# Performance work log

Hardware: AMD Instinct MI355X
Metric: run time of the kernel (lower is better)

## Reference

```python
import jax, jax.numpy as jnp
import numpy as np

H = 96
W = 96
FX = 96.0
FY = 96.0
NEAR = 0.3
EPS = 1e-8


def q2r(quat):
    # quat: [N,4] (w,x,y,z) -> [N,3,3]
    q = quat / (jnp.linalg.norm(quat, axis=-1, keepdims=True) + 1e-12)
    w, x, y, z = q[:, 0], q[:, 1], q[:, 2], q[:, 3]
    R = jnp.stack([
        1 - 2 * (y * y + z * z), 2 * (x * y - w * z), 2 * (x * z + w * y),
        2 * (x * y + w * z), 1 - 2 * (x * x + z * z), 2 * (y * z - w * x),
        2 * (x * z - w * y), 2 * (y * z + w * x), 1 - 2 * (x * x + y * y),
    ], axis=-1).reshape(-1, 3, 3)
    return R


def setup_inputs() -> dict:
    key = jax.random.key(0)
    ks = jax.random.split(key, 8)
    N = 4096
    pos_xy = jax.random.uniform(ks[0], (N, 2), minval=-2.0, maxval=2.0, dtype=jnp.float32)
    pos_z = jax.random.uniform(ks[1], (N, 1), minval=2.0, maxval=6.0, dtype=jnp.float32)
    pos = jnp.concatenate([pos_xy, pos_z], axis=-1)
    rgb = jax.random.normal(ks[2], (N, 3), dtype=jnp.float32)
    opa = jax.random.normal(ks[3], (N,), dtype=jnp.float32)
    quat = jax.random.normal(ks[4], (N, 4), dtype=jnp.float32)
    scale = jax.random.uniform(ks[5], (N, 3), dtype=jnp.float32) * 0.05 + 0.005
    rot = jnp.eye(3, dtype=jnp.float32)
    tran = jnp.zeros(3, dtype=jnp.float32)
    return {"pos": pos, "rgb": rgb, "opa": opa, "quat": quat, "scale": scale, "rot": rot, "tran": tran}


def reference(pos, rgb, opa, quat, scale, rot, tran):
    # ---- project: world -> camera -> image space ----
    cam = pos @ rot.T + tran[None, :]              # [N,3]
    x, y, z = cam[:, 0], cam[:, 1], cam[:, 2]
    r = jnp.linalg.norm(cam, axis=-1)              # depth = ray length (camera_to_image)
    mean2d = jnp.stack([x / z, y / z], axis=-1)    # [N,2]

    # jacobian of (x/z, y/z, |p|) wrt camera-space point, [N,3,3]
    zeros = jnp.zeros_like(z)
    J = jnp.stack([
        1.0 / z, zeros, -x / (z * z),
        zeros, 1.0 / z, -y / (z * z),
        x / r, y / r, z / r,
    ], axis=-1).reshape(-1, 3, 3)

    # ---- 3D covariance: R S S^T R^T ----
    R = q2r(quat)                                   # [N,3,3]
    s = jnp.abs(scale) + 1e-4                       # [N,3]
    RS = R * s[:, None, :]                          # R @ diag(s)
    cov3d = jnp.einsum('nij,nkj->nik', RS, RS)      # [N,3,3]

    # ---- 2D covariance: (J W) cov3d (J W)^T, upper-left 2x2 ----
    JW = jnp.einsum('nij,jk->nik', J, rot)          # [N,3,3]
    cov2d = jnp.einsum('nij,njk,nlk->nil', JW, cov3d, JW)[:, :2, :2]  # [N,2,2]

    a = cov2d[:, 0, 0] + EPS
    d = cov2d[:, 1, 1] + EPS
    b = 0.5 * (cov2d[:, 0, 1] + cov2d[:, 1, 0])
    det = a * d - b * b
    inv_a = d / det
    inv_b = -b / det
    inv_d = a / det

    rgb_act = jax.nn.sigmoid(rgb)                   # [N,3]
    opa_act = jax.nn.sigmoid(opa)                   # [N]

    # ---- per-pixel gaussian evaluation in normalized image space ----
    u = (jnp.arange(W, dtype=jnp.float32) + 0.5 - W / 2) / FX   # [W]
    v = (jnp.arange(H, dtype=jnp.float32) + 0.5 - H / 2) / FY   # [H]
    pu = jnp.tile(u, H)                                          # [P]
    pv = jnp.repeat(v, W)                                        # [P]

    dx = pu[None, :] - mean2d[:, 0:1]               # [N,P]
    dy = pv[None, :] - mean2d[:, 1:2]               # [N,P]
    power = -0.5 * (inv_a[:, None] * dx * dx + 2.0 * inv_b[:, None] * dx * dy + inv_d[:, None] * dy * dy)
    alpha = opa_act[:, None] * jnp.exp(power)       # [N,P]
    alpha = jnp.clip(alpha, 0.0, 0.99)
    valid = (z > NEAR).astype(alpha.dtype)[:, None]
    alpha = alpha * valid

    # ---- depth-sorted alpha compositing ----
    order = jnp.argsort(r)                          # near -> far
    alpha_s = alpha[order]                          # [N,P]
    rgb_s = rgb_act[order]                          # [N,3]

    log_1m = jnp.log1p(-alpha_s)                    # [N,P]
    cum = jnp.cumsum(log_1m, axis=0)
    logT = jnp.concatenate([jnp.zeros((1, alpha_s.shape[1]), alpha_s.dtype), cum[:-1]], axis=0)
    w = jnp.exp(logT) * alpha_s                     # [N,P] blending weights
    img = jnp.einsum('np,nc->pc', w, rgb_s)         # [P,3]
    return img.reshape(H, W, 3)
```

## Files before the change

kernel.cpp:

```cpp
#include <hip/hip_runtime.h>
#include <math.h>

#define N_G   4096
#define IMW   96
#define TILE  6
#define TILES_X 16
#define NTILE (TILES_X*TILES_X)
#define NTHR  1024
#define NW    (NTHR/64)
#define NST   (N_G/NTHR)
#define NPX   (TILE*TILE)
#define NSEG  16
#define BCAP  2048
#define CAP   512
#define FXI   (1.0f/96.0f)
#define NEARP 0.3f
#define EPSV  1e-8f
#define LOG2E 1.4426950408889634f
#define LN2   0.6931471805599453f
#define CULL_K 26.0f

typedef unsigned long long ull;
typedef __attribute__((ext_vector_type(2))) unsigned long long ull2;

__global__ __launch_bounds__(NTHR, 1) void splat_k(
    const float* __restrict__ pos, const float* __restrict__ rgb,
    const float* __restrict__ opa, const float* __restrict__ quat,
    const float* __restrict__ scale, const float* __restrict__ rot,
    const float* __restrict__ tran, float* __restrict__ out)
{
    __shared__ unsigned int bl[BCAP];
    __shared__ __align__(16) ull skey[CAP+2];
    __shared__ int sslot[CAP];
    __shared__ float4 g0[CAP], g1[CAP];
    __shared__ float  g2[CAP];
    __shared__ float4 pix[NSEG*NPX];
    __shared__ int psum[4][CAP];
    __shared__ int bcnt_sh, cnt_sh;

    const int t = threadIdx.x;
    const int tile = blockIdx.x;
    const int tx = tile % TILES_X, ty = tile / TILES_X;
    const float u0 = ((float)(tx*TILE) + 0.5f - 48.0f) * FXI;
    const float u1 = u0 + (TILE-1) * FXI;
    const float v0 = ((float)(ty*TILE) + 0.5f - 48.0f) * FXI;
    const float v1 = v0 + (TILE-1) * FXI;
    const int wid = t >> 6, lane = t & 63;

    if (t == 0) { bcnt_sh = 0; cnt_sh = 0; }

    float R00=rot[0],R01=rot[1],R02=rot[2];
    float R10=rot[3],R11=rot[4],R12=rot[5];
    float R20=rot[6],R21=rot[7],R22=rot[8];
    float t0=tran[0], t1=tran[1], t2=tran[2];

    float pp0[NST], pp1[NST], pp2[NST], po[NST], ps0[NST], ps1[NST], ps2[NST];
    #pragma unroll
    for (int st = 0; st < NST; st++) {
        int gi = st*NTHR + t;
        pp0[st]=pos[gi*3+0]; pp1[st]=pos[gi*3+1]; pp2[st]=pos[gi*3+2];
        po[st]=opa[gi];
        ps0[st]=scale[gi*3+0]; ps1[st]=scale[gi*3+1]; ps2[st]=scale[gi*3+2];
    }
    __syncthreads();

    #pragma unroll
    for (int st = 0; st < NST; st++) {
        int gi = st*NTHR + t;
        float x = R00*pp0[st] + R01*pp1[st] + R02*pp2[st] + t0;
        float y = R10*pp0[st] + R11*pp1[st] + R12*pp2[st] + t1;
        float z = R20*pp0[st] + R21*pp1[st] + R22*pp2[st] + t2;
        float invz = 1.0f/z;
        float mu = x*invz, mv = y*invz;

        float inz2 = invz*invz;
        float fn = 2.0f*inz2 + (x*x + y*y)*inz2*inz2;
        float smax = fmaxf(fmaxf(fabsf(ps0[st]), fabsf(ps1[st])), fabsf(ps2[st])) + 1e-4f;
        float lmax = fn*smax*smax + EPSV;
        float amp = CULL_K + 1.0f + fminf(0.0f, po[st]*LOG2E);
        float r2b = amp * lmax * (2.0f*LN2) * 1.02f;

        float cu = fminf(fmaxf(mu, u0), u1);
        float cv = fminf(fmaxf(mv, v0), v1);
        float ddx = mu - cu, ddy = mv - cv;
        bool flag = (z > NEARP) && (amp > 0.0f) && (ddx*ddx + ddy*ddy <= r2b);

        ull m = __ballot(flag);
        int nm = __popcll(m);
        int base = 0;
        if (lane == 0 && nm) base = atomicAdd(&bcnt_sh, nm);
        base = __shfl(base, 0);
        if (flag) {
            int p = base + __popcll(m & ((1ull << lane) - 1ull));
            if (p < BCAP) bl[p] = (unsigned int)gi;
        }
    }
    __syncthreads();
    int bcnt = bcnt_sh; if (bcnt > BCAP) bcnt = BCAP;

    for (int s0i = 0; s0i < bcnt; s0i += NTHR) {
        int s = s0i + t;
        bool flag = false;
        float4 o0, o1; float ocb = 0.0f, rr = 0.0f;
        unsigned int gi = 0;
        if (s < bcnt) {
            gi = bl[s];
            float p0=pos[gi*3+0], p1=pos[gi*3+1], p2=pos[gi*3+2];
            float x = R00*p0 + R01*p1 + R02*p2 + t0;
            float y = R10*p0 + R11*p1 + R12*p2 + t1;
            float z = R20*p0 + R21*p1 + R22*p2 + t2;
            rr = sqrtf(x*x + y*y + z*z);
            float invz = 1.0f/z;
            float mu = x*invz, mv = y*invz;

            float J02 = -x*invz*invz, J12 = -y*invz*invz;
            float JW00 = invz*R00 + J02*R20;
            float JW01 = invz*R01 + J02*R21;
            float JW02 = invz*R02 + J02*R22;
            float JW10 = invz*R10 + J12*R20;
            float JW11 = invz*R11 + J12*R21;
            float JW12 = invz*R12 + J12*R22;

            float qw=quat[gi*4+0], qx=quat[gi*4+1], qy=quat[gi*4+2], qz=quat[gi*4+3];
            float qn = sqrtf(qw*qw+qx*qx+qy*qy+qz*qz) + 1e-12f;
            float qi = 1.0f/qn;
            qw*=qi; qx*=qi; qy*=qi; qz*=qi;
            float Q00=1.f-2.f*(qy*qy+qz*qz), Q01=2.f*(qx*qy-qw*qz), Q02=2.f*(qx*qz+qw*qy);
            float Q10=2.f*(qx*qy+qw*qz), Q11=1.f-2.f*(qx*qx+qz*qz), Q12=2.f*(qy*qz-qw*qx);
            float Q20=2.f*(qx*qz-qw*qy), Q21=2.f*(qy*qz+qw*qx), Q22=1.f-2.f*(qx*qx+qy*qy);

            float sa=fabsf(scale[gi*3+0])+1e-4f;
            float sb=fabsf(scale[gi*3+1])+1e-4f;
            float sc=fabsf(scale[gi*3+2])+1e-4f;
            float A00=Q00*sa,A01=Q01*sb,A02=Q02*sc;
            float A10=Q10*sa,A11=Q11*sb,A12=Q12*sc;
            float A20=Q20*sa,A21=Q21*sb,A22=Q22*sc;
            float C00=A00*A00+A01*A01+A02*A02;
            float C01=A00*A10+A01*A11+A02*A12;
            float C02=A00*A20+A01*A21+A02*A22;
            float C11=A10*A10+A11*A11+A12*A12;
            float C12=A10*A20+A11*A21+A12*A22;
            float C22=A20*A20+A21*A21+A22*A22;
            float M00=JW00*C00+JW01*C01+JW02*C02;
            float M01=JW00*C01+JW01*C11+JW02*C12;
            float M02=JW00*C02+JW01*C12+JW02*C22;
            float M10=JW10*C00+JW11*C01+JW12*C02;
            float M11=JW10*C01+JW11*C11+JW12*C12;
            float M12=JW10*C02+JW11*C12+JW12*C22;
            float a  = M00*JW00+M01*JW01+M02*JW02 + EPSV;
            float d  = M10*JW10+M11*JW11+M12*JW12 + EPSV;
            float bb = 0.5f*((M00*JW10+M01*JW11+M02*JW12)+(M10*JW00+M11*JW01+M12*JW02));
            float invdet = 1.0f/(a*d - bb*bb);
            float iaP = -0.5f*d*invdet*LOG2E;
            float ibP =  bb*invdet*LOG2E;
            float idP = -0.5f*a*invdet*LOG2E;

            float sig_o = 1.0f/(1.0f+__expf(-opa[gi]));
            float opa_eff = (z > NEARP) ? sig_o : 0.0f;

            float q00 = -iaP, q01 = -0.5f*ibP, q11 = -idP;
            float df = q00 - q11;
            float lam = 0.5f*((q00 + q11) - sqrtf(df*df + 4.0f*q01*q01));
            lam = fmaxf(lam, 1e-20f);
            float r2 = (CULL_K + log2f(opa_eff)) / lam;

            float cu = fminf(fmaxf(mu, u0), u1);
            float cv = fminf(fmaxf(mv, v0), v1);
            float ddx = mu - cu, ddy = mv - cv;
            flag = (ddx*ddx + ddy*ddy) <= r2;

            if (flag) {
                float c0 = 1.0f/(1.0f+__expf(-rgb[gi*3+0]));
                float c1 = 1.0f/(1.0f+__expf(-rgb[gi*3+1]));
                float c2 = 1.0f/(1.0f+__expf(-rgb[gi*3+2]));
                o0 = make_float4(mu, mv, iaP, ibP);
                o1 = make_float4(idP, opa_eff, c0, c1);
                ocb = c2;
            }
        }
        ull m = __ballot(flag);
        int nm = __popcll(m);
        int base = 0;
        if (lane == 0 && nm) base = atomicAdd(&cnt_sh, nm);
        base = __shfl(base, 0);
        if (flag) {
            int p = base + __popcll(m & ((1ull << lane) - 1ull));
            if (p < CAP) {
                g0[p] = o0; g1[p] = o1; g2[p] = ocb;
                skey[p] = ((ull)__float_as_uint(rr) << 32) | gi;
            }
        }
    }
    __syncthreads();
    int cnt = cnt_sh; if (cnt > CAP) cnt = CAP;

    if (t == 0 && (cnt & 1)) skey[cnt] = ~0ull;
    __syncthreads();
    int cnt2 = cnt + (cnt & 1);
    int nq = cnt2 >> 1;
    const ull2* sk2 = (const ull2*)skey;
    ull v = 0;
    bool small = (cnt <= 256);
    if (small) {
        const int g = t >> 8, e = t & 255;
        if (e < cnt) {
            v = skey[e];
            int wA = (nq * g) >> 2;
            int wB = (nq * (g+1)) >> 2;
            int c = 0;
            for (int w = wA; w < wB; w++) {
                ull2 p = sk2[w];
                c += (p.x < v) ? 1 : 0;
                c += (p.y < v) ? 1 : 0;
            }
            psum[g][e] = c;
        }
    } else {
        const int g = t >> 9, e = t & 511;
        if (e < cnt) {
            v = skey[e];
            int wA = (nq * g) >> 1;
            int wB = (nq * (g+1)) >> 1;
            int c = 0;
            for (int w = wA; w < wB; w++) {
                ull2 p = sk2[w];
                c += (p.x < v) ? 1 : 0;
                c += (p.y < v) ? 1 : 0;
            }
            psum[g][e] = c;
        }
    }
    __syncthreads();
    if (t < cnt) {
        int r = small ? (psum[0][t] + psum[1][t] + psum[2][t] + psum[3][t])
                      : (psum[0][t] + psum[1][t]);
        skey[r]  = v;
        sslot[r] = t;
    }
    __syncthreads();

    {
        const int seg = wid;
        const bool act = (lane < NPX);
        const int pid = act ? lane : 0;
        const int px = tx*TILE + (pid % TILE);
        const int py = ty*TILE + (pid / TILE);
        const float pu = ((float)px + 0.5f - 48.0f) * FXI;
        const float pv = ((float)py + 0.5f - 48.0f) * FXI;

        const int per = (cnt + NSEG - 1) / NSEG;
        const int sA = min(seg * per, cnt);
        const int sB = min(sA + per, cnt);

        float T = 1.0f, cr = 0.0f, cg = 0.0f, cb = 0.0f;
        for (int s = sA; s < sB; s++) {
            int slot = sslot[s];
            float4 a0 = g0[slot];
            float4 a1 = g1[slot];
            float  a2 = g2[slot];
            float dx = pu - a0.x;
            float dy = pv - a0.y;
            float pw = dx*(a0.z*dx + a0.w*dy) + a1.x*dy*dy;
            float al = fminf(a1.y * __builtin_amdgcn_exp2f(pw), 0.99f);
            float w = T * al;
            cr += w * a1.z;
            cg += w * a1.w;
            cb += w * a2;
            T *= (1.0f - al);
        }
        if (act) pix[seg*NPX + pid] = make_float4(cr, cg, cb, T);
    }
    __syncthreads();

    if (t < NPX) {
        float orr = 0.0f, og = 0.0f, ob = 0.0f, T2 = 1.0f;
        #pragma unroll
        for (int s = 0; s < NSEG; s++) {
            float4 P = pix[s*NPX + t];
            orr += T2 * P.x;
            og  += T2 * P.y;
            ob  += T2 * P.z;
            T2  *= P.w;
        }
        int px = tx*TILE + (t % TILE);
        int py = ty*TILE + (t / TILE);
        int pixel = py * IMW + px;
        out[pixel*3+0] = orr;
        out[pixel*3+1] = og;
        out[pixel*3+2] = ob;
    }
}

extern "C" void kernel_launch(void* const* d_in, const int* in_sizes, int n_in,
                              void* d_out, int out_size, void* d_ws, size_t ws_size,
                              hipStream_t stream) {
    const float* pos   = (const float*)d_in[0];
    const float* rgb   = (const float*)d_in[1];
    const float* opa   = (const float*)d_in[2];
    const float* quat  = (const float*)d_in[3];
    const float* scale = (const float*)d_in[4];
    const float* rot   = (const float*)d_in[5];
    const float* tran  = (const float*)d_in[6];
    float* out = (float*)d_out;

    splat_k<<<NTILE, NTHR, 0, stream>>>(pos, rgb, opa, quat, scale, rot, tran, out);
}
```

Baseline: 14.22 us.

## Cull gaussians with exact ellipse bounding box and unify rank sort

The tile culling test now compares the per-axis extent of each gaussian's ellipse (from the quadratic form's determinant) against the per-axis distance to the tile. This replaces the circle bounded by the smallest eigenvalue, dropping a sqrt and keeping fewer elongated gaussians per tile. The counting rank sort now always uses four partial-sum groups, with each thread ranking two keys, replacing the two-mode small/large branch. This trades more compare work per thread for a better split of the key list when counts are large. The psum array must hold 512 entries per group for the new indexing to be safe.

```diff
diff --git a/kernel.cpp b/kernel.cpp
--- a/kernel.cpp
+++ b/kernel.cpp
@@ -159,15 +159,13 @@
             float opa_eff = (z > NEARP) ? sig_o : 0.0f;
 
             float q00 = -iaP, q01 = -0.5f*ibP, q11 = -idP;
-            float df = q00 - q11;
-            float lam = 0.5f*((q00 + q11) - sqrtf(df*df + 4.0f*q01*q01));
-            lam = fmaxf(lam, 1e-20f);
-            float r2 = (CULL_K + log2f(opa_eff)) / lam;
+            float detQ = q00*q11 - q01*q01;
+            float K = CULL_K + log2f(opa_eff);
 
             float cu = fminf(fmaxf(mu, u0), u1);
             float cv = fminf(fmaxf(mv, v0), v1);
             float ddx = mu - cu, ddy = mv - cv;
-            flag = (ddx*ddx + ddy*ddy) <= r2;
+            flag = (ddx*ddx*detQ <= K*q11) && (ddy*ddy*detQ <= K*q00);
 
             if (flag) {
                 float c0 = 1.0f/(1.0f+__expf(-rgb[gi*3+0]));
@@ -199,43 +197,36 @@
     int cnt2 = cnt + (cnt & 1);
     int nq = cnt2 >> 1;
     const ull2* sk2 = (const ull2*)skey;
-    ull v = 0;
-    bool small = (cnt <= 256);
-    if (small) {
-        const int g = t >> 8, e = t & 255;
-        if (e < cnt) {
-            v = skey[e];
-            int wA = (nq * g) >> 2;
-            int wB = (nq * (g+1)) >> 2;
-            int c = 0;
-            for (int w = wA; w < wB; w++) {
-                ull2 p = sk2[w];
-                c += (p.x < v) ? 1 : 0;
-                c += (p.y < v) ? 1 : 0;
-            }
-            psum[g][e] = c;
-        }
-    } else {
-        const int g = t >> 9, e = t & 511;
-        if (e < cnt) {
-            v = skey[e];
-            int wA = (nq * g) >> 1;
-            int wB = (nq * (g+1)) >> 1;
-            int c = 0;
-            for (int w = wA; w < wB; w++) {
-                ull2 p = sk2[w];
-                c += (p.x < v) ? 1 : 0;
-                c += (p.y < v) ? 1 : 0;
-            }
-            psum[g][e] = c;
-        }
-    }
-    __syncthreads();
-    if (t < cnt) {
-        int r = small ? (psum[0][t] + psum[1][t] + psum[2][t] + psum[3][t])
-                      : (psum[0][t] + psum[1][t]);
-        skey[r]  = v;
-        sslot[r] = t;
+    const int g = t >> 8, e = t & 255;
+    const bool h1 = (e < cnt), h2 = (e + 256 < cnt);
+    ull kv1 = 0, kv2 = 0;
+    if (h1) {
+        kv1 = skey[e];
+        if (h2) kv2 = skey[e + 256];
+        int wA = (nq * g) >> 2;
+        int wB = (nq * (g+1)) >> 2;
+        int c1 = 0, c2 = 0;
+        for (int w = wA; w < wB; w++) {
+            ull2 p = sk2[w];
+            c1 += (p.x < kv1) ? 1 : 0;
+            c1 += (p.y < kv1) ? 1 : 0;
+            c2 += (p.x < kv2) ? 1 : 0;
+            c2 += (p.y < kv2) ? 1 : 0;
+        }
+        psum[g][e] = c1;
+        if (h2) psum[g][e + 256] = c2;
+    }
+    __syncthreads();
+    if (t < 256 && h1) {
+        int r1 = psum[0][e] + psum[1][e] + psum[2][e] + psum[3][e];
+        skey[r1]  = kv1;
+        sslot[r1] = e;
+        if (h2) {
+            int e2 = e + 256;
+            int r2 = psum[0][e2] + psum[1][e2] + psum[2][e2] + psum[3][e2];
+            skey[r2]  = kv2;
+            sslot[r2] = e2;
+        }
     }
     __syncthreads();
 
```

Measured after the change: 14.02 us. No clear change (-1.4%).
